# Kernel tuning notes

Hardware: AMD Instinct MI355X
Metric: run time of the kernel (lower is better)

The kernel has to match this reference:

```python
import jax, jax.numpy as jnp
import numpy as np

EPS = 1e-3  # matches module default eps=0.001


def setup_inputs() -> dict:
    key = jax.random.key(0)
    k1, k2 = jax.random.split(key)
    B, C, W, H = 8, 64, 496, 432  # KITTI BEV grid, pillar feature dim 64
    x = jax.random.normal(k1, (B, C, W, H), dtype=jnp.float32)
    # are exactly zero across all channels so x.sum(1) == 0 there.
    occ = (jax.random.uniform(k2, (B, W, H)) < 0.10).astype(jnp.float32)
    x = x * occ[:, None, :, :]
    return {"x": x}


def reference(x):
    # Faithful to the torch module, including its padding artifact: each batch's
    # nonzero index list is padded to N = max(num_nonzeros) with index (0,0), so
    # padded slots gather x[b,:,0,0], contribute to mean/var with multiplicity
    # (N - n_b), and scatter a normalized value back into pixel (0,0).
    B, C, Wd, Hd = x.shape
    mask = (x.sum(axis=1) != 0)                 # [B,W,H] occupied pixels
    n = mask.sum(axis=(1, 2))                    # [B] nonzeros per batch
    N = n.max()                                  # padded gather length
    pad = (N - n).astype(x.dtype)                # [B] number of (0,0) pad slots
    x00 = x[:, :, 0, 0]                          # [B,C] value gathered by pads
    mb = mask[:, None, :, :].astype(x.dtype)     # [B,1,W,H]

    count = (B * N).astype(x.dtype)              # total gathered entries
    total = (x * mb).sum(axis=(0, 2, 3)) + (pad[:, None] * x00).sum(axis=0)  # [C]
    mean = total / count                         # [C]

    d = x - mean[None, :, None, None]
    sq = ((d * d) * mb).sum(axis=(0, 2, 3)) + (pad[:, None] * (x00 - mean) ** 2).sum(axis=0)
    var = sq / count                             # [C] biased variance (mean over gathered)

    inv = 1.0 / jnp.sqrt(var + EPS)              # [C]; note: mean is NOT subtracted
    out = jnp.where(mask[:, None, :, :], x * inv[None, :, None, None], x)

    # scatter-back hits (0,0) whenever batch b had pad slots OR (0,0) was nonzero
    write00 = (pad > 0) | mask[:, 0, 0]          # [B]
    out = out.at[:, :, 0, 0].set(
        jnp.where(write00[:, None], x00 * inv[None, :], out[:, :, 0, 0])
    )
    return out
```

## Files before the change

kernel.cpp:

```cpp
#include <hip/hip_runtime.h>

#define WH      214272
#define GPB     53568
#define TOTAL4  (512*GPB)
#define CHUNKS  (TOTAL4/64)
#define CPP     (GPB/64)

#define BLOCKS  2048
#define NW      (BLOCKS*4)
#define PER     ((CHUNKS + NW - 1)/NW)
#define NTCH    25

#define NREP    16
#define WS_FLOATS (NREP*64*2 + 64)

typedef float floatx4 __attribute__((ext_vector_type(4)));

template<bool NT>
__device__ __forceinline__ void sweep(const floatx4* __restrict__ base, int lo, int hi,
                                      float& s0, float& s1, float& s2, float& s3,
                                      float& q0, float& q1, float& q2, float& q3,
                                      int& cnt, const bool isC0) {
    int k = hi;
    while (k - 6 >= lo) {
        k -= 6;
        floatx4 v0, v1, v2, v3, v4, v5;
        if (NT) {
            v0 = __builtin_nontemporal_load(&base[(size_t)(k + 5) * 64]);
            v1 = __builtin_nontemporal_load(&base[(size_t)(k + 4) * 64]);
            v2 = __builtin_nontemporal_load(&base[(size_t)(k + 3) * 64]);
            v3 = __builtin_nontemporal_load(&base[(size_t)(k + 2) * 64]);
            v4 = __builtin_nontemporal_load(&base[(size_t)(k + 1) * 64]);
            v5 = __builtin_nontemporal_load(&base[(size_t)(k + 0) * 64]);
        } else {
            v0 = base[(size_t)(k + 5) * 64];
            v1 = base[(size_t)(k + 4) * 64];
            v2 = base[(size_t)(k + 3) * 64];
            v3 = base[(size_t)(k + 2) * 64];
            v4 = base[(size_t)(k + 1) * 64];
            v5 = base[(size_t)(k + 0) * 64];
        }
        s0 += (v0.x + v0.y) + (v0.z + v0.w);
        s1 += (v1.x + v1.y) + (v1.z + v1.w);
        s2 += (v2.x + v2.y) + (v2.z + v2.w);
        s3 += (v3.x + v3.y) + (v3.z + v3.w);
        q0 = fmaf(v0.w, v0.w, fmaf(v0.z, v0.z, fmaf(v0.y, v0.y, fmaf(v0.x, v0.x, q0))));
        q1 = fmaf(v1.w, v1.w, fmaf(v1.z, v1.z, fmaf(v1.y, v1.y, fmaf(v1.x, v1.x, q1))));
        q2 = fmaf(v2.w, v2.w, fmaf(v2.z, v2.z, fmaf(v2.y, v2.y, fmaf(v2.x, v2.x, q2))));
        q3 = fmaf(v3.w, v3.w, fmaf(v3.z, v3.z, fmaf(v3.y, v3.y, fmaf(v3.x, v3.x, q3))));
        s0 += (v4.x + v4.y) + (v4.z + v4.w);
        s1 += (v5.x + v5.y) + (v5.z + v5.w);
        q0 = fmaf(v4.w, v4.w, fmaf(v4.z, v4.z, fmaf(v4.y, v4.y, fmaf(v4.x, v4.x, q0))));
        q1 = fmaf(v5.w, v5.w, fmaf(v5.z, v5.z, fmaf(v5.y, v5.y, fmaf(v5.x, v5.x, q1))));
        if (isC0) {
            cnt += (v0.x != 0.f) + (v0.y != 0.f) + (v0.z != 0.f) + (v0.w != 0.f);
            cnt += (v1.x != 0.f) + (v1.y != 0.f) + (v1.z != 0.f) + (v1.w != 0.f);
            cnt += (v2.x != 0.f) + (v2.y != 0.f) + (v2.z != 0.f) + (v2.w != 0.f);
            cnt += (v3.x != 0.f) + (v3.y != 0.f) + (v3.z != 0.f) + (v3.w != 0.f);
            cnt += (v4.x != 0.f) + (v4.y != 0.f) + (v4.z != 0.f) + (v4.w != 0.f);
            cnt += (v5.x != 0.f) + (v5.y != 0.f) + (v5.z != 0.f) + (v5.w != 0.f);
        }
    }
    while (k > lo) {
        --k;
        floatx4 v;
        if (NT) v = __builtin_nontemporal_load(&base[(size_t)k * 64]);
        else    v = base[(size_t)k * 64];
        s0 += (v.x + v.y) + (v.z + v.w);
        q0 = fmaf(v.w, v.w, fmaf(v.z, v.z, fmaf(v.y, v.y, fmaf(v.x, v.x, q0))));
        if (isC0) cnt += (v.x != 0.f) + (v.y != 0.f) + (v.z != 0.f) + (v.w != 0.f);
    }
}

__global__ __launch_bounds__(256, 8) void k_stats(const floatx4* __restrict__ x4,
                                                  float* __restrict__ gsum,
                                                  float* __restrict__ gsq,
                                                  int* __restrict__ gn) {
    const int lane = threadIdx.x & 63;
    const int gw   = blockIdx.x * 4 + (threadIdx.x >> 6);
    const int rep  = gw & (NREP - 1);
    const int c0   = gw * PER;
    const int c1   = min(c0 + PER, CHUNKS);
    if (c0 >= c1) return;
    const int split = c0 + NTCH;
    const floatx4* base = x4 + lane;

    int e = c1;
    while (e > c0) {
        const int plane = (int)((unsigned)(e - 1) / CPP);
        const int s = max(c0, plane * CPP);
        const bool isC0 = (plane & 63) == 0;

        float s0 = 0.f, s1 = 0.f, s2 = 0.f, s3 = 0.f;
        float q0 = 0.f, q1 = 0.f, q2 = 0.f, q3 = 0.f;
        int cnt = 0;

        const int pl = max(s, split);
        if (e > pl)
            sweep<false>(base, pl, e, s0, s1, s2, s3, q0, q1, q2, q3, cnt, isC0);
        const int nthi = min(e, split);
        if (nthi > s)
            sweep<true>(base, s, nthi, s0, s1, s2, s3, q0, q1, q2, q3, cnt, isC0);

        float ss = (s0 + s1) + (s2 + s3);
        float qq = (q0 + q1) + (q2 + q3);
#pragma unroll
        for (int m = 1; m < 64; m <<= 1) {
            ss += __shfl_xor(ss, m, 64);
            qq += __shfl_xor(qq, m, 64);
        }
        if (isC0) {
#pragma unroll
            for (int m = 1; m < 64; m <<= 1) cnt += __shfl_xor(cnt, m, 64);
        }
        if (lane == 0) {
            atomicAdd(&gsum[rep * 64 + (plane & 63)], ss);
            atomicAdd(&gsq[rep * 64 + (plane & 63)], qq);
            if (isC0) atomicAdd(&gn[(rep & 7) * 8 + (plane >> 6)], cnt);
        }
        e = s;
    }
}

__global__ __launch_bounds__(256, 8) void k_scale(const floatx4* __restrict__ x4,
                                                  floatx4* __restrict__ out4,
                                                  const float* __restrict__ gsum,
                                                  const float* __restrict__ gsq,
                                                  const int* __restrict__ gn) {
    __shared__ float sinv[64];
    const int tid = threadIdx.x;
    if (tid < 64) {
        const int c = tid;
        const float* x = (const float*)x4;
        float total = 0.f, S2 = 0.f;
#pragma unroll
        for (int r = 0; r < NREP; ++r) {
            total += gsum[r * 64 + c];
            S2    += gsq[r * 64 + c];
        }
        int nb[8];
        int N = 0;
#pragma unroll
        for (int b = 0; b < 8; ++b) {
            int v = 0;
#pragma unroll
            for (int r = 0; r < 8; ++r) v += gn[r * 8 + b];
            nb[b] = v;
            N = max(N, v);
        }
#pragma unroll
        for (int b = 0; b < 8; ++b) {
            const float pad = (float)(N - nb[b]);
            const float x00 = x[(size_t)(b * 64 + c) * WH];
            total = fmaf(pad, x00, total);
            S2    = fmaf(pad, x00 * x00, S2);
        }
        const float count = (float)(8 * N);
        const float mean  = total / count;
        const float var   = S2 / count - mean * mean;
        sinv[c] = 1.0f / sqrtf(var + 0.001f);
    }
    __syncthreads();

    const int lane = tid & 63;
    const int gw   = blockIdx.x * 4 + (tid >> 6);
    const int c0   = gw * PER;
    const int c1   = min(c0 + PER, CHUNKS);
#pragma unroll 4
    for (int ch = c1 - 1; ch >= c0; --ch) {
        const int plane = (int)((unsigned)ch / CPP);
        const float inv = sinv[plane & 63];
        const size_t i = (size_t)ch * 64 + lane;
        floatx4 v = __builtin_nontemporal_load(&x4[i]);
        v.x *= inv; v.y *= inv; v.z *= inv; v.w *= inv;
        __builtin_nontemporal_store(v, &out4[i]);
    }
}

extern "C" void kernel_launch(void* const* d_in, const int* in_sizes, int n_in,
                              void* d_out, int out_size, void* d_ws, size_t ws_size,
                              hipStream_t stream) {
    const float* x  = (const float*)d_in[0];
    float* out      = (float*)d_out;
    float* wsf      = (float*)d_ws;
    float* gsum     = wsf;
    float* gsq      = wsf + NREP * 64;
    int*   gn       = (int*)(wsf + NREP * 128);

    (void)hipMemsetAsync(d_ws, 0, WS_FLOATS * sizeof(float), stream);

    k_stats<<<BLOCKS, 256, 0, stream>>>((const floatx4*)x, gsum, gsq, gn);
    k_scale<<<BLOCKS, 256, 0, stream>>>((const floatx4*)x, (floatx4*)out,
                                        gsum, gsq, gn);
}
```

Baseline: 760.9 us.

## Interleave stats chunks across block waves and drop reverse/nontemporal sweep

The stats kernel now gives each block a contiguous range of 212 chunks, with its four waves taking interleaved chunks (stride 4) instead of each wave sweeping its own contiguous range backwards. The reverse-order traversal and the nontemporal-load prefix, which were meant to leave data in cache for the scale pass, are removed, and every block range is assumed to span at most two channel planes. This changes DRAM access locality within a block and gives up the cache-retention trick between the two kernels. The scale kernel still uses the old per-wave PER partition, but PER is now hardcoded to 53, so its coverage depends on that constant.

Measured after the change: 763.4 us. No clear change (+0.3%).

```diff
diff --git a/kernel.cpp b/kernel.cpp
--- a/kernel.cpp
+++ b/kernel.cpp
@@ -7,39 +7,26 @@
 #define CPP     (GPB/64)
 
 #define BLOCKS  2048
-#define NW      (BLOCKS*4)
-#define PER     ((CHUNKS + NW - 1)/NW)
-#define NTCH    25
+#define PER     53
+#define BPB     (4*PER)
 
 #define NREP    16
 #define WS_FLOATS (NREP*64*2 + 64)
 
 typedef float floatx4 __attribute__((ext_vector_type(4)));
 
-template<bool NT>
-__device__ __forceinline__ void sweep(const floatx4* __restrict__ base, int lo, int hi,
-                                      float& s0, float& s1, float& s2, float& s3,
-                                      float& q0, float& q1, float& q2, float& q3,
-                                      int& cnt, const bool isC0) {
-    int k = hi;
-    while (k - 6 >= lo) {
-        k -= 6;
-        floatx4 v0, v1, v2, v3, v4, v5;
-        if (NT) {
-            v0 = __builtin_nontemporal_load(&base[(size_t)(k + 5) * 64]);
-            v1 = __builtin_nontemporal_load(&base[(size_t)(k + 4) * 64]);
-            v2 = __builtin_nontemporal_load(&base[(size_t)(k + 3) * 64]);
-            v3 = __builtin_nontemporal_load(&base[(size_t)(k + 2) * 64]);
-            v4 = __builtin_nontemporal_load(&base[(size_t)(k + 1) * 64]);
-            v5 = __builtin_nontemporal_load(&base[(size_t)(k + 0) * 64]);
-        } else {
-            v0 = base[(size_t)(k + 5) * 64];
-            v1 = base[(size_t)(k + 4) * 64];
-            v2 = base[(size_t)(k + 3) * 64];
-            v3 = base[(size_t)(k + 2) * 64];
-            v4 = base[(size_t)(k + 1) * 64];
-            v5 = base[(size_t)(k + 0) * 64];
-        }
+__device__ __forceinline__ void sweep4(const floatx4* __restrict__ p, int jlo, int jhi,
+                                       float& s0, float& s1, float& s2, float& s3,
+                                       float& q0, float& q1, float& q2, float& q3,
+                                       int& cnt, const bool isC0) {
+    int j = jlo;
+    for (; j + 6 <= jhi; j += 6) {
+        const floatx4 v0 = p[(size_t)(j + 0) * 256];
+        const floatx4 v1 = p[(size_t)(j + 1) * 256];
+        const floatx4 v2 = p[(size_t)(j + 2) * 256];
+        const floatx4 v3 = p[(size_t)(j + 3) * 256];
+        const floatx4 v4 = p[(size_t)(j + 4) * 256];
+        const floatx4 v5 = p[(size_t)(j + 5) * 256];
         s0 += (v0.x + v0.y) + (v0.z + v0.w);
         s1 += (v1.x + v1.y) + (v1.z + v1.w);
         s2 += (v2.x + v2.y) + (v2.z + v2.w);
@@ -61,11 +48,8 @@
             cnt += (v5.x != 0.f) + (v5.y != 0.f) + (v5.z != 0.f) + (v5.w != 0.f);
         }
     }
-    while (k > lo) {
-        --k;
-        floatx4 v;
-        if (NT) v = __builtin_nontemporal_load(&base[(size_t)k * 64]);
-        else    v = base[(size_t)k * 64];
+    for (; j < jhi; ++j) {
+        const floatx4 v = p[(size_t)j * 256];
         s0 += (v.x + v.y) + (v.z + v.w);
         q0 = fmaf(v.w, v.w, fmaf(v.z, v.z, fmaf(v.y, v.y, fmaf(v.x, v.x, q0))));
         if (isC0) cnt += (v.x != 0.f) + (v.y != 0.f) + (v.z != 0.f) + (v.w != 0.f);
@@ -77,30 +61,34 @@
                                                   float* __restrict__ gsq,
                                                   int* __restrict__ gn) {
     const int lane = threadIdx.x & 63;
-    const int gw   = blockIdx.x * 4 + (threadIdx.x >> 6);
+    const int w    = threadIdx.x >> 6;
+    const int gw   = blockIdx.x * 4 + w;
     const int rep  = gw & (NREP - 1);
-    const int c0   = gw * PER;
-    const int c1   = min(c0 + PER, CHUNKS);
-    if (c0 >= c1) return;
-    const int split = c0 + NTCH;
-    const floatx4* base = x4 + lane;
+    const int bs   = blockIdx.x * BPB;
+    const int be   = min(bs + BPB, CHUNKS);
+    const int start = bs + w;
+    if (start >= be) return;
+    const int nj = ((be - start) + 3) >> 2;
 
-    int e = c1;
-    while (e > c0) {
-        const int plane = (int)((unsigned)(e - 1) / CPP);
-        const int s = max(c0, plane * CPP);
+    const int pA = (int)((unsigned)bs / CPP);
+    const int cB = (pA + 1) * CPP;
+    int jb = (cB <= start) ? 0 : ((cB - start + 3) >> 2);
+    if (jb > nj) jb = nj;
+
+    const floatx4* p = x4 + (size_t)start * 64 + lane;
+
+#pragma unroll
+    for (int seg = 0; seg < 2; ++seg) {
+        const int jlo = seg ? jb : 0;
+        const int jhi = seg ? nj : jb;
+        if (jlo >= jhi) continue;
+        const int plane = pA + seg;
         const bool isC0 = (plane & 63) == 0;
 
         float s0 = 0.f, s1 = 0.f, s2 = 0.f, s3 = 0.f;
         float q0 = 0.f, q1 = 0.f, q2 = 0.f, q3 = 0.f;
         int cnt = 0;
-
-        const int pl = max(s, split);
-        if (e > pl)
-            sweep<false>(base, pl, e, s0, s1, s2, s3, q0, q1, q2, q3, cnt, isC0);
-        const int nthi = min(e, split);
-        if (nthi > s)
-            sweep<true>(base, s, nthi, s0, s1, s2, s3, q0, q1, q2, q3, cnt, isC0);
+        sweep4(p, jlo, jhi, s0, s1, s2, s3, q0, q1, q2, q3, cnt, isC0);
 
         float ss = (s0 + s1) + (s2 + s3);
         float qq = (q0 + q1) + (q2 + q3);
@@ -118,7 +106,6 @@
             atomicAdd(&gsq[rep * 64 + (plane & 63)], qq);
             if (isC0) atomicAdd(&gn[(rep & 7) * 8 + (plane >> 6)], cnt);
         }
-        e = s;
     }
 }
 
```
